# Kernel optimization log

Hardware: AMD Instinct MI355X
Metric: run time of the kernel (lower is better)

The kernel has to match this reference:

```python
import jax, jax.numpy as jnp
import numpy as np

B, N, D = 8192, 512, 3

def setup_inputs() -> dict:
    key = jax.random.key(0)
    k1, k2 = jax.random.split(key)
    inp = jax.random.normal(k1, (B, N, D), dtype=jnp.float32)
    tgt = jax.random.normal(k2, (B, N, D), dtype=jnp.float32)
    return {"input": inp, "target": tgt}

def _kabsch_rotation(x, y):
    # x, y: (B, N, 3) centered. Covariance C: (B, 3, 3)
    C = jnp.einsum('bji,bjk->bik', x, y)
    U, _, Vh = jnp.linalg.svd(C, full_matrices=False)
    d = jnp.linalg.det(U) * jnp.linalg.det(Vh)  # (B,)
    # flip sign of last row of Vh where det is negative (proper rotation)
    Vh = Vh.at[:, -1, :].multiply(d[:, None])
    return U @ Vh  # (B, 3, 3)

def reference(input, target):
    x = input - input.mean(-2, keepdims=True)
    y = target - target.mean(-2, keepdims=True)
    R = _kabsch_rotation(x, y)
    aligned = jnp.einsum('bnd,bde->bne', x, R)
    return jnp.mean((aligned - y) ** 2)
```

## Files before the change

kernel.cpp:

```cpp
#include <hip/hip_runtime.h>
#include <math.h>

#define B_TOT 8192
#define N_PTS 512

__global__ __launch_bounds__(128) void kabsch_batch(const float* __restrict__ x,
                                                    const float* __restrict__ y,
                                                    float* __restrict__ ws)
{
    const int b = blockIdx.x;
    const int t = threadIdx.x;
    const float4* xb = reinterpret_cast<const float4*>(x) + (size_t)b * 384;
    const float4* yb = reinterpret_cast<const float4*>(y) + (size_t)b * 384;

    float4 fx0 = xb[3*t+0], fx1 = xb[3*t+1], fx2 = xb[3*t+2];
    float4 fy0 = yb[3*t+0], fy1 = yb[3*t+1], fy2 = yb[3*t+2];

    float px[4][3] = {{fx0.x,fx0.y,fx0.z},{fx0.w,fx1.x,fx1.y},
                      {fx1.z,fx1.w,fx2.x},{fx2.y,fx2.z,fx2.w}};
    float py[4][3] = {{fy0.x,fy0.y,fy0.z},{fy0.w,fy1.x,fy1.y},
                      {fy1.z,fy1.w,fy2.x},{fy2.y,fy2.z,fy2.w}};

    float acc[17];
    #pragma unroll
    for (int k = 0; k < 17; k++) acc[k] = 0.f;

    #pragma unroll
    for (int p = 0; p < 4; p++) {
        #pragma unroll
        for (int d = 0; d < 3; d++) {
            float xv = px[p][d], yv = py[p][d];
            acc[d]     += xv;
            acc[3 + d] += yv;
            acc[15]    += xv * xv;
            acc[16]    += yv * yv;
            #pragma unroll
            for (int e = 0; e < 3; e++)
                acc[6 + d*3 + e] += xv * py[p][e];
        }
    }

    #pragma unroll
    for (int k = 0; k < 17; k++) {
        #pragma unroll
        for (int off = 32; off; off >>= 1)
            acc[k] += __shfl_down(acc[k], off, 64);
    }

    __shared__ float red[2][17];
    const int wave = t >> 6, lane = t & 63;
    if (lane == 0) {
        #pragma unroll
        for (int k = 0; k < 17; k++) red[wave][k] = acc[k];
    }
    __syncthreads();

    if (t == 0) {
        double S[17];
        #pragma unroll
        for (int k = 0; k < 17; k++) S[k] = (double)red[0][k] + (double)red[1][k];

        const double Nn = (double)N_PTS;
        double mx[3] = {S[0]/Nn, S[1]/Nn, S[2]/Nn};
        double my[3] = {S[3]/Nn, S[4]/Nn, S[5]/Nn};

        double C[3][3];
        for (int d = 0; d < 3; d++)
            for (int e = 0; e < 3; e++)
                C[d][e] = S[6 + d*3 + e] - Nn * mx[d] * my[e];

        double sxx = S[15] - Nn*(mx[0]*mx[0] + mx[1]*mx[1] + mx[2]*mx[2]);
        double syy = S[16] - Nn*(my[0]*my[0] + my[1]*my[1] + my[2]*my[2]);

        double K00=0,K01=0,K02=0,K11=0,K12=0,K22=0;
        for (int k = 0; k < 3; k++) {
            K00 += C[k][0]*C[k][0]; K01 += C[k][0]*C[k][1]; K02 += C[k][0]*C[k][2];
            K11 += C[k][1]*C[k][1]; K12 += C[k][1]*C[k][2]; K22 += C[k][2]*C[k][2];
        }

        double q3 = (K00 + K11 + K22) / 3.0;
        double p1 = K01*K01 + K02*K02 + K12*K12;
        double a00 = K00 - q3, a11 = K11 - q3, a22 = K22 - q3;
        double p2 = a00*a00 + a11*a11 + a22*a22 + 2.0*p1;
        double lam1, lam2, lam3;
        if (p2 <= 1e-300) {
            lam1 = lam2 = lam3 = q3;
        } else {
            double pp  = sqrt(p2 / 6.0);
            double ip  = 1.0 / pp;
            double b00 = a00*ip, b11 = a11*ip, b22 = a22*ip;
            double b01 = K01*ip, b02 = K02*ip, b12 = K12*ip;
            double detB = b00*(b11*b22 - b12*b12)
                        - b01*(b01*b22 - b12*b02)
                        + b02*(b01*b12 - b11*b02);
            double r = 0.5 * detB;
            r = fmin(1.0, fmax(-1.0, r));
            double phi = acos(r) / 3.0;
            lam1 = q3 + 2.0*pp*cos(phi);
            lam3 = q3 + 2.0*pp*cos(phi + 2.0943951023931954923);
            lam2 = 3.0*q3 - lam1 - lam3;
        }
        lam1 = fmax(lam1, 0.0); lam2 = fmax(lam2, 0.0); lam3 = fmax(lam3, 0.0);
        double s1 = sqrt(lam1), s2 = sqrt(lam2), s3 = sqrt(lam3);

        double detC = C[0][0]*(C[1][1]*C[2][2] - C[1][2]*C[2][1])
                    - C[0][1]*(C[1][0]*C[2][2] - C[1][2]*C[2][0])
                    + C[0][2]*(C[1][0]*C[2][1] - C[1][1]*C[2][0]);
        double sgn = (detC < 0.0) ? -1.0 : 1.0;
        double trRC = s1 + s2 + sgn * s3;

        ws[b] = (float)(sxx + syy - 2.0 * trRC);
    }
}

__global__ __launch_bounds__(256) void reduce_final(const float* __restrict__ ws,
                                                    float* __restrict__ out)
{
    double s = 0.0;
    for (int i = threadIdx.x; i < B_TOT; i += 256) s += (double)ws[i];
    #pragma unroll
    for (int off = 32; off; off >>= 1) s += __shfl_down(s, off, 64);
    __shared__ double red[4];
    const int wave = threadIdx.x >> 6, lane = threadIdx.x & 63;
    if (lane == 0) red[wave] = s;
    __syncthreads();
    if (threadIdx.x == 0) {
        double tot = red[0] + red[1] + red[2] + red[3];
        out[0] = (float)(tot / ((double)B_TOT * (double)N_PTS * 3.0));
    }
}

extern "C" void kernel_launch(void* const* d_in, const int* in_sizes, int n_in,
                              void* d_out, int out_size, void* d_ws, size_t ws_size,
                              hipStream_t stream) {
    const float* x = (const float*)d_in[0];
    const float* y = (const float*)d_in[1];
    float* out = (float*)d_out;
    float* ws  = (float*)d_ws;

    kabsch_batch<<<B_TOT, 128, 0, stream>>>(x, y, ws);
    reduce_final<<<1, 256, 0, stream>>>(ws, out);
}
```

Before: 124.2 us.

## Split per-batch sums from 3x3 eigen-solve into separate thread-parallel kernel

```diff
diff --git a/kernel.cpp b/kernel.cpp
--- a/kernel.cpp
+++ b/kernel.cpp
@@ -3,41 +3,39 @@
 
 #define B_TOT 8192
 #define N_PTS 512
+#define WAVES_PER_BLOCK 4
+#define BLK_A (64 * WAVES_PER_BLOCK)
 
-__global__ __launch_bounds__(128) void kabsch_batch(const float* __restrict__ x,
-                                                    const float* __restrict__ y,
-                                                    float* __restrict__ ws)
+__global__ __launch_bounds__(BLK_A) void sums_kernel(const float* __restrict__ x,
+                                                     const float* __restrict__ y,
+                                                     float* __restrict__ ws)
 {
-    const int b = blockIdx.x;
-    const int t = threadIdx.x;
-    const float4* xb = reinterpret_cast<const float4*>(x) + (size_t)b * 384;
-    const float4* yb = reinterpret_cast<const float4*>(y) + (size_t)b * 384;
+    const int wave = threadIdx.x >> 6;
+    const int lane = threadIdx.x & 63;
+    const int b = blockIdx.x * WAVES_PER_BLOCK + wave;
 
-    float4 fx0 = xb[3*t+0], fx1 = xb[3*t+1], fx2 = xb[3*t+2];
-    float4 fy0 = yb[3*t+0], fy1 = yb[3*t+1], fy2 = yb[3*t+2];
+    const float4* xb = reinterpret_cast<const float4*>(x) + (size_t)b * 384 + 6 * lane;
+    const float4* yb = reinterpret_cast<const float4*>(y) + (size_t)b * 384 + 6 * lane;
 
-    float px[4][3] = {{fx0.x,fx0.y,fx0.z},{fx0.w,fx1.x,fx1.y},
-                      {fx1.z,fx1.w,fx2.x},{fx2.y,fx2.z,fx2.w}};
-    float py[4][3] = {{fy0.x,fy0.y,fy0.z},{fy0.w,fy1.x,fy1.y},
-                      {fy1.z,fy1.w,fy2.x},{fy2.y,fy2.z,fy2.w}};
+    union { float4 v[6]; float f[24]; } X, Y;
+    #pragma unroll
+    for (int i = 0; i < 6; i++) { X.v[i] = xb[i]; Y.v[i] = yb[i]; }
 
     float acc[17];
     #pragma unroll
     for (int k = 0; k < 17; k++) acc[k] = 0.f;
 
     #pragma unroll
-    for (int p = 0; p < 4; p++) {
-        #pragma unroll
-        for (int d = 0; d < 3; d++) {
-            float xv = px[p][d], yv = py[p][d];
-            acc[d]     += xv;
-            acc[3 + d] += yv;
-            acc[15]    += xv * xv;
-            acc[16]    += yv * yv;
-            #pragma unroll
-            for (int e = 0; e < 3; e++)
-                acc[6 + d*3 + e] += xv * py[p][e];
-        }
+    for (int p = 0; p < 8; p++) {
+        float x0 = X.f[3*p], x1 = X.f[3*p+1], x2 = X.f[3*p+2];
+        float y0 = Y.f[3*p], y1 = Y.f[3*p+1], y2 = Y.f[3*p+2];
+        acc[0] += x0;  acc[1] += x1;  acc[2] += x2;
+        acc[3] += y0;  acc[4] += y1;  acc[5] += y2;
+        acc[6]  += x0*y0; acc[7]  += x0*y1; acc[8]  += x0*y2;
+        acc[9]  += x1*y0; acc[10] += x1*y1; acc[11] += x1*y2;
+        acc[12] += x2*y0; acc[13] += x2*y1; acc[14] += x2*y2;
+        acc[15] += x0*x0 + x1*x1 + x2*x2;
+        acc[16] += y0*y0 + y1*y1 + y2*y2;
     }
 
     #pragma unroll
@@ -47,87 +45,94 @@
             acc[k] += __shfl_down(acc[k], off, 64);
     }
 
-    __shared__ float red[2][17];
-    const int wave = t >> 6, lane = t & 63;
     if (lane == 0) {
         #pragma unroll
-        for (int k = 0; k < 17; k++) red[wave][k] = acc[k];
-    }
-    __syncthreads();
-
-    if (t == 0) {
-        double S[17];
-        #pragma unroll
-        for (int k = 0; k < 17; k++) S[k] = (double)red[0][k] + (double)red[1][k];
-
-        const double Nn = (double)N_PTS;
-        double mx[3] = {S[0]/Nn, S[1]/Nn, S[2]/Nn};
-        double my[3] = {S[3]/Nn, S[4]/Nn, S[5]/Nn};
-
-        double C[3][3];
-        for (int d = 0; d < 3; d++)
-            for (int e = 0; e < 3; e++)
-                C[d][e] = S[6 + d*3 + e] - Nn * mx[d] * my[e];
-
-        double sxx = S[15] - Nn*(mx[0]*mx[0] + mx[1]*mx[1] + mx[2]*mx[2]);
-        double syy = S[16] - Nn*(my[0]*my[0] + my[1]*my[1] + my[2]*my[2]);
-
-        double K00=0,K01=0,K02=0,K11=0,K12=0,K22=0;
-        for (int k = 0; k < 3; k++) {
-            K00 += C[k][0]*C[k][0]; K01 += C[k][0]*C[k][1]; K02 += C[k][0]*C[k][2];
-            K11 += C[k][1]*C[k][1]; K12 += C[k][1]*C[k][2]; K22 += C[k][2]*C[k][2];
-        }
-
-        double q3 = (K00 + K11 + K22) / 3.0;
-        double p1 = K01*K01 + K02*K02 + K12*K12;
-        double a00 = K00 - q3, a11 = K11 - q3, a22 = K22 - q3;
-        double p2 = a00*a00 + a11*a11 + a22*a22 + 2.0*p1;
-        double lam1, lam2, lam3;
-        if (p2 <= 1e-300) {
-            lam1 = lam2 = lam3 = q3;
-        } else {
-            double pp  = sqrt(p2 / 6.0);
-            double ip  = 1.0 / pp;
-            double b00 = a00*ip, b11 = a11*ip, b22 = a22*ip;
-            double b01 = K01*ip, b02 = K02*ip, b12 = K12*ip;
-            double detB = b00*(b11*b22 - b12*b12)
-                        - b01*(b01*b22 - b12*b02)
-                        + b02*(b01*b12 - b11*b02);
-            double r = 0.5 * detB;
-            r = fmin(1.0, fmax(-1.0, r));
-            double phi = acos(r) / 3.0;
-            lam1 = q3 + 2.0*pp*cos(phi);
-            lam3 = q3 + 2.0*pp*cos(phi + 2.0943951023931954923);
-            lam2 = 3.0*q3 - lam1 - lam3;
-        }
-        lam1 = fmax(lam1, 0.0); lam2 = fmax(lam2, 0.0); lam3 = fmax(lam3, 0.0);
-        double s1 = sqrt(lam1), s2 = sqrt(lam2), s3 = sqrt(lam3);
-
-        double detC = C[0][0]*(C[1][1]*C[2][2] - C[1][2]*C[2][1])
-                    - C[0][1]*(C[1][0]*C[2][2] - C[1][2]*C[2][0])
-                    + C[0][2]*(C[1][0]*C[2][1] - C[1][1]*C[2][0]);
-        double sgn = (detC < 0.0) ? -1.0 : 1.0;
-        double trRC = s1 + s2 + sgn * s3;
-
-        ws[b] = (float)(sxx + syy - 2.0 * trRC);
+        for (int k = 0; k < 17; k++) ws[k * B_TOT + b] = acc[k];
     }
 }
 
-__global__ __launch_bounds__(256) void reduce_final(const float* __restrict__ ws,
-                                                    float* __restrict__ out)
+__global__ __launch_bounds__(256) void solve_kernel(const float* __restrict__ ws,
+                                                    double* __restrict__ blockSums)
 {
-    double s = 0.0;
-    for (int i = threadIdx.x; i < B_TOT; i += 256) s += (double)ws[i];
+    const int b = blockIdx.x * 256 + threadIdx.x;
+
+    double S[17];
     #pragma unroll
-    for (int off = 32; off; off >>= 1) s += __shfl_down(s, off, 64);
+    for (int k = 0; k < 17; k++) S[k] = (double)ws[k * B_TOT + b];
+
+    const double Nn = (double)N_PTS;
+    double mx[3] = {S[0]/Nn, S[1]/Nn, S[2]/Nn};
+    double my[3] = {S[3]/Nn, S[4]/Nn, S[5]/Nn};
+
+    double C[3][3];
+    #pragma unroll
+    for (int d = 0; d < 3; d++)
+        #pragma unroll
+        for (int e = 0; e < 3; e++)
+            C[d][e] = S[6 + d*3 + e] - Nn * mx[d] * my[e];
+
+    double sxx = S[15] - Nn*(mx[0]*mx[0] + mx[1]*mx[1] + mx[2]*mx[2]);
+    double syy = S[16] - Nn*(my[0]*my[0] + my[1]*my[1] + my[2]*my[2]);
+
+    double K00=0,K01=0,K02=0,K11=0,K12=0,K22=0;
+    #pragma unroll
+    for (int k = 0; k < 3; k++) {
+        K00 += C[k][0]*C[k][0]; K01 += C[k][0]*C[k][1]; K02 += C[k][0]*C[k][2];
+        K11 += C[k][1]*C[k][1]; K12 += C[k][1]*C[k][2]; K22 += C[k][2]*C[k][2];
+    }
+
+    double q3 = (K00 + K11 + K22) / 3.0;
+    double p1 = K01*K01 + K02*K02 + K12*K12;
+    double a00 = K00 - q3, a11 = K11 - q3, a22 = K22 - q3;
+    double p2 = a00*a00 + a11*a11 + a22*a22 + 2.0*p1;
+    double lam1, lam2, lam3;
+    if (p2 <= 1e-300) {
+        lam1 = lam2 = lam3 = q3;
+    } else {
+        double pp  = sqrt(p2 / 6.0);
+        double ip  = 1.0 / pp;
+        double b00 = a00*ip, b11 = a11*ip, b22 = a22*ip;
+        double b01 = K01*ip, b02 = K02*ip, b12 = K12*ip;
+        double detB = b00*(b11*b22 - b12*b12)
+                    - b01*(b01*b22 - b12*b02)
+                    + b02*(b01*b12 - b11*b02);
+        double r = 0.5 * detB;
+        r = fmin(1.0, fmax(-1.0, r));
+        double phi = acos(r) / 3.0;
+        lam1 = q3 + 2.0*pp*cos(phi);
+        lam3 = q3 + 2.0*pp*cos(phi + 2.0943951023931954923);
+        lam2 = 3.0*q3 - lam1 - lam3;
+    }
+    lam1 = fmax(lam1, 0.0); lam2 = fmax(lam2, 0.0); lam3 = fmax(lam3, 0.0);
+    double s1 = sqrt(lam1), s2 = sqrt(lam2), s3 = sqrt(lam3);
+
+    double detC = C[0][0]*(C[1][1]*C[2][2] - C[1][2]*C[2][1])
+                - C[0][1]*(C[1][0]*C[2][2] - C[1][2]*C[2][0])
+                + C[0][2]*(C[1][0]*C[2][1] - C[1][1]*C[2][0]);
+    double sgn = (detC < 0.0) ? -1.0 : 1.0;
+    double trRC = s1 + s2 + sgn * s3;
+
+    double v = sxx + syy - 2.0 * trRC;
+
+    #pragma unroll
+    for (int off = 32; off; off >>= 1) v += __shfl_down(v, off, 64);
     __shared__ double red[4];
     const int wave = threadIdx.x >> 6, lane = threadIdx.x & 63;
-    if (lane == 0) red[wave] = s;
+    if (lane == 0) red[wave] = v;
     __syncthreads();
-    if (threadIdx.x == 0) {
-        double tot = red[0] + red[1] + red[2] + red[3];
-        out[0] = (float)(tot / ((double)B_TOT * (double)N_PTS * 3.0));
-    }
+    if (threadIdx.x == 0)
+        blockSums[blockIdx.x] = red[0] + red[1] + red[2] + red[3];
+}
+
+__global__ __launch_bounds__(64) void final_kernel(const double* __restrict__ bs,
+                                                   float* __restrict__ out)
+{
+    const int t = threadIdx.x;
+    double v = (t < 32) ? bs[t] : 0.0;
+    #pragma unroll
+    for (int off = 32; off; off >>= 1) v += __shfl_down(v, off, 64);
+    if (t == 0)
+        out[0] = (float)(v / ((double)B_TOT * (double)N_PTS * 3.0));
 }
 
 extern "C" void kernel_launch(void* const* d_in, const int* in_sizes, int n_in,
@@ -136,8 +141,11 @@
     const float* x = (const float*)d_in[0];
     const float* y = (const float*)d_in[1];
     float* out = (float*)d_out;
-    float* ws  = (float*)d_ws;
 
-    kabsch_batch<<<B_TOT, 128, 0, stream>>>(x, y, ws);
-    reduce_final<<<1, 256, 0, stream>>>(ws, out);
+    float*  ws = (float*)d_ws;
+    double* bs = (double*)((char*)d_ws + 17 * B_TOT * 4);
+
+    sums_kernel <<<B_TOT / WAVES_PER_BLOCK, BLK_A, 0, stream>>>(x, y, ws);
+    solve_kernel<<<B_TOT / 256, 256, 0, stream>>>(ws, bs);
+    final_kernel<<<1, 64, 0, stream>>>(bs, out);
 }
```

After: 123.4 us. Within noise of the previous version (-0.6%).
